# Kernel tuning notes

Hardware: AMD Instinct MI355X
Metric: run time of the kernel (lower is better)

Reference implementation:

```python
import jax, jax.numpy as jnp
import numpy as np

D_MODEL = 768
CTX_DIM = 1024
N_HEAD = 12
N_QUERIES = 256
DIM_HEAD = D_MODEL // N_HEAD  # 64
INNER = DIM_HEAD * N_HEAD     # 768
EPS = 1e-5


def layernorm(x, w, b):
    mu = jnp.mean(x, axis=-1, keepdims=True)
    var = jnp.mean((x - mu) ** 2, axis=-1, keepdims=True)
    return (x - mu) * jax.lax.rsqrt(var + EPS) * w + b


def setup_inputs() -> dict:
    key = jax.random.key(0)
    ks = jax.random.split(key, 9)
    x = jax.random.normal(ks[0], (8, 4096, CTX_DIM), dtype=jnp.float32)
    query = jax.random.normal(ks[1], (N_QUERIES, D_MODEL), dtype=jnp.float32)
    # Linear weights stored [in, out] (y = x @ W)
    Wq = jax.random.normal(ks[2], (D_MODEL, INNER), dtype=jnp.float32) * 0.02
    Wkv = jax.random.normal(ks[3], (CTX_DIM, 2 * INNER), dtype=jnp.float32) * 0.02
    Wout = jax.random.normal(ks[4], (INNER, D_MODEL), dtype=jnp.float32) * 0.02
    ln_q_w = jnp.ones((D_MODEL,), jnp.float32)
    ln_q_b = jnp.zeros((D_MODEL,), jnp.float32)
    ln_k_w = jnp.ones((CTX_DIM,), jnp.float32)
    ln_k_b = jnp.zeros((CTX_DIM,), jnp.float32)
    return {"x": x, "query": query, "ln_q_w": ln_q_w, "ln_q_b": ln_q_b,
            "ln_k_w": ln_k_w, "ln_k_b": ln_k_b, "Wq": Wq, "Wkv": Wkv, "Wout": Wout}


def reference(x, query, ln_q_w, ln_q_b, ln_k_w, ln_k_b, Wq, Wkv, Wout):
    b = x.shape[0]
    h, dh = N_HEAD, DIM_HEAD
    scale = dh ** -0.5
    xk = x[:, None]  # b 1 n d  (m = 1)
    m, n = xk.shape[1], xk.shape[2]
    q = jnp.broadcast_to(query, (b, m) + query.shape)  # b m nq d
    xk = layernorm(xk, ln_k_w, ln_k_b)
    q = layernorm(q, ln_q_w, ln_q_b)
    q = q @ Wq                          # b m nq inner
    kv = xk @ Wkv                       # b m n 2*inner
    k, v = jnp.split(kv, 2, axis=-1)
    def split_heads(t):
        bb, tt, nn, _ = t.shape
        return t.reshape(bb, tt, nn, h, dh).transpose(0, 3, 1, 2, 4)  # b h t n dh
    q, k, v = split_heads(q), split_heads(k), split_heads(v)
    sim = jnp.einsum('bhtid,bhtjd->bhtij', q * scale, k)
    attn = jax.nn.softmax(sim, axis=-1)
    out = jnp.einsum('bhtij,bhtjd->bhtid', attn, v)  # b h t nq dh
    out = out.transpose(0, 2, 3, 1, 4).reshape(b, m, N_QUERIES, INNER)
    return (out @ Wout).squeeze(axis=1)  # b nq d_model
```

## Files before the change

### kernel.cpp

```cpp
#include <hip/hip_runtime.h>
#include <hip/hip_bf16.h>
#include <math.h>

#define B_    8
#define T_    4096
#define CD    1024
#define DM    768
#define NH    12
#define DH    64
#define NQ    256
#define INNER 768
#define NKV   1536
#define MKV   (B_*T_)
#define EPS   1e-5f
#define SCALE 0.125f

typedef __attribute__((ext_vector_type(8))) short short8;
typedef __attribute__((ext_vector_type(4))) float f32x4;

__device__ __forceinline__ unsigned short f2bf(float f) {
  union { __hip_bfloat16 h; unsigned short u; } cv;
  cv.h = __float2bfloat16(f);
  return cv.u;
}

__global__ __launch_bounds__(256) void tb32_kernel(
    const float* __restrict__ src, unsigned short* __restrict__ dst,
    int Cn, int R) {
  __shared__ float tile[32][33];
  int k0 = blockIdx.x * 32, n0 = blockIdx.y * 32;
  int tid = threadIdx.x;
  int r = tid >> 3, c4 = (tid & 7) * 4;
  float4 v = *reinterpret_cast<const float4*>(&src[(size_t)(k0 + r) * Cn + n0 + c4]);
  tile[r][c4 + 0] = v.x; tile[r][c4 + 1] = v.y; tile[r][c4 + 2] = v.z; tile[r][c4 + 3] = v.w;
  __syncthreads();
  ushort4 o4;
  o4.x = f2bf(tile[c4 + 0][r]);
  o4.y = f2bf(tile[c4 + 1][r]);
  o4.z = f2bf(tile[c4 + 2][r]);
  o4.w = f2bf(tile[c4 + 3][r]);
  *reinterpret_cast<ushort4*>(&dst[(size_t)(n0 + r) * R + k0 + c4]) = o4;
}

__global__ __launch_bounds__(256) void qln_kernel(
    const float* __restrict__ query, const float* __restrict__ lnw,
    const float* __restrict__ lnb, unsigned short* __restrict__ qn) {
  int row = blockIdx.x, tid = threadIdx.x;
  __shared__ float rbuf[256];
  const float* qr = query + (size_t)row * DM;
  float v0 = qr[tid], v1 = qr[tid + 256], v2 = qr[tid + 512];
  rbuf[tid] = v0 + v1 + v2;
  __syncthreads();
  for (int o = 128; o > 0; o >>= 1) { if (tid < o) rbuf[tid] += rbuf[tid + o]; __syncthreads(); }
  float mean = rbuf[0] * (1.f / 768.f);
  __syncthreads();
  float d0 = v0 - mean, d1 = v1 - mean, d2 = v2 - mean;
  rbuf[tid] = d0 * d0 + d1 * d1 + d2 * d2;
  __syncthreads();
  for (int o = 128; o > 0; o >>= 1) { if (tid < o) rbuf[tid] += rbuf[tid + o]; __syncthreads(); }
  float var = rbuf[0] * (1.f / 768.f);
  float rs = rsqrtf(var + EPS);
  unsigned short* dst = qn + (size_t)row * DM;
  dst[tid]       = f2bf(d0 * rs * lnw[tid]       + lnb[tid]);
  dst[tid + 256] = f2bf(d1 * rs * lnw[tid + 256] + lnb[tid + 256]);
  dst[tid + 512] = f2bf(d2 * rs * lnw[tid + 512] + lnb[tid + 512]);
}

__global__ __launch_bounds__(256) void xnorm_kernel(
    const float* __restrict__ x, const float* __restrict__ lnw,
    const float* __restrict__ lnb, unsigned short* __restrict__ xn) {
  int row = blockIdx.x, tid = threadIdx.x;
  float4 v = reinterpret_cast<const float4*>(x + (size_t)row * CD)[tid];
  float s  = v.x + v.y + v.z + v.w;
  float ss = v.x * v.x + v.y * v.y + v.z * v.z + v.w * v.w;
  #pragma unroll
  for (int o = 32; o > 0; o >>= 1) { s += __shfl_down(s, o); ss += __shfl_down(ss, o); }
  __shared__ float sm[8];
  int wid = tid >> 6, lane = tid & 63;
  if (lane == 0) { sm[wid] = s; sm[4 + wid] = ss; }
  __syncthreads();
  float S  = sm[0] + sm[1] + sm[2] + sm[3];
  float SS = sm[4] + sm[5] + sm[6] + sm[7];
  float m  = S * (1.f / 1024.f);
  float var = SS * (1.f / 1024.f) - m * m;
  float rs = rsqrtf(fmaxf(var, 0.f) + EPS);
  float4 wv = reinterpret_cast<const float4*>(lnw)[tid];
  float4 bv = reinterpret_cast<const float4*>(lnb)[tid];
  ushort4 o4;
  o4.x = f2bf((v.x - m) * rs * wv.x + bv.x);
  o4.y = f2bf((v.y - m) * rs * wv.y + bv.y);
  o4.z = f2bf((v.z - m) * rs * wv.z + bv.z);
  o4.w = f2bf((v.w - m) * rs * wv.w + bv.w);
  reinterpret_cast<ushort4*>(xn + (size_t)row * CD)[tid] = o4;
}

template <int MODE>
__global__ __launch_bounds__(256) void gemm128_kernel(
    const unsigned short* __restrict__ A, const unsigned short* __restrict__ Bt,
    void* __restrict__ Cout, int N, int K, int nN, float scale, int swz) {
  __shared__ __attribute__((aligned(16))) unsigned short As[128 * 64];
  __shared__ __attribute__((aligned(16))) unsigned short Bs[128 * 64];
  int tid = threadIdx.x;
  int w = tid >> 6, lane = tid & 63;
  int bid = blockIdx.x;
  int sw = swz ? ((bid & 7) * ((int)gridDim.x >> 3) + (bid >> 3)) : bid;
  int mt = sw / nN, nt = sw % nN;
  int m0 = mt * 128, n0 = nt * 128;

  int srow[4], skoff[4];
  #pragma unroll
  for (int i = 0; i < 4; ++i) {
    int L = w * 4096 + i * 1024 + lane * 16;
    int row = L >> 7;
    int slot = (L >> 4) & 7;
    srow[i] = row;
    skoff[i] = ((slot ^ (row & 7)) << 3);
  }

  f32x4 acc[4][4];
  #pragma unroll
  for (int m = 0; m < 4; ++m)
    #pragma unroll
    for (int n = 0; n < 4; ++n) acc[m][n] = (f32x4){0.f, 0.f, 0.f, 0.f};

  int wr = w >> 1, wc = w & 1;
  int l15 = lane & 15, l4 = lane >> 4;

  for (int t = 0; t < K / 64; ++t) {
    int k0 = t * 64;
    #pragma unroll
    for (int i = 0; i < 4; ++i) {
      __builtin_amdgcn_global_load_lds(
          (const __attribute__((address_space(1))) void*)(A + (size_t)(m0 + srow[i]) * K + k0 + skoff[i]),
          (__attribute__((address_space(3))) void*)(As + w * 2048 + i * 512 + lane * 8),
          16, 0, 0);
    }
    #pragma unroll
    for (int i = 0; i < 4; ++i) {
      __builtin_amdgcn_global_load_lds(
          (const __attribute__((address_space(1))) void*)(Bt + (size_t)(n0 + srow[i]) * K + k0 + skoff[i]),
          (__attribute__((address_space(3))) void*)(Bs + w * 2048 + i * 512 + lane * 8),
          16, 0, 0);
    }
    __syncthreads();
    #pragma unroll
    for (int kh = 0; kh < 2; ++kh) {
      short8 af[4], bf[4];
      #pragma unroll
      for (int m = 0; m < 4; ++m) {
        int row = wr * 64 + m * 16 + l15;
        int byte = row * 128 + (((l4 + 4 * kh) ^ (row & 7)) << 4);
        af[m] = *reinterpret_cast<const short8*>(reinterpret_cast<const char*>(As) + byte);
      }
      #pragma unroll
      for (int n = 0; n < 4; ++n) {
        int row = wc * 64 + n * 16 + l15;
        int byte = row * 128 + (((l4 + 4 * kh) ^ (row & 7)) << 4);
        bf[n] = *reinterpret_cast<const short8*>(reinterpret_cast<const char*>(Bs) + byte);
      }
      #pragma unroll
      for (int m = 0; m < 4; ++m)
        #pragma unroll
        for (int n = 0; n < 4; ++n)
          acc[m][n] = __builtin_amdgcn_mfma_f32_16x16x32_bf16(af[m], bf[n], acc[m][n], 0, 0, 0);
    }
    __syncthreads();
  }

  #pragma unroll
  for (int m = 0; m < 4; ++m) {
    int grow = m0 + wr * 64 + m * 16 + l4 * 4;
    #pragma unroll
    for (int n = 0; n < 4; ++n) {
      int gcol = n0 + wc * 64 + n * 16 + l15;
      #pragma unroll
      for (int r = 0; r < 4; ++r) {
        if (MODE == 0)
          ((unsigned short*)Cout)[(size_t)(grow + r) * N + gcol] = f2bf(acc[m][n][r] * scale);
        else
          ((float*)Cout)[(size_t)(grow + r) * N + gcol] = acc[m][n][r];
      }
    }
  }
}

#define KBM 256
#define KBN 256
#define KBK 64
__global__ __launch_bounds__(512, 2) void kv_split_kernel(
    const unsigned short* __restrict__ xn, const unsigned short* __restrict__ wkvT,
    unsigned short* __restrict__ kvbK, unsigned short* __restrict__ vT) {
  __shared__ __attribute__((aligned(16))) unsigned short As[2][KBM * KBK];
  __shared__ __attribute__((aligned(16))) unsigned short Bs[2][KBN * KBK];
  int tid = threadIdx.x;
  int w = tid >> 6, lane = tid & 63;
  int wm = w >> 2, wn = w & 3;
  int l15 = lane & 15, l4 = lane >> 4;

  int bid = blockIdx.x;
  int sw = (bid & 7) * 96 + (bid >> 3);
  int mt = sw / (NKV / KBN), nt = sw % (NKV / KBN);
  int m0 = mt * KBM, n0 = nt * KBN;

  int srow[4], koff[4];
  #pragma unroll
  for (int i = 0; i < 4; ++i) {
    int r = i * 64 + (tid >> 3);
    srow[i] = r;
    koff[i] = (((tid & 7) ^ (r & 7)) << 3);
  }

  f32x4 acc[8][4];
  #pragma unroll
  for (int m = 0; m < 8; ++m)
    #pragma unroll
    for (int n = 0; n < 4; ++n) acc[m][n] = (f32x4){0.f, 0.f, 0.f, 0.f};

  #pragma unroll
  for (int i = 0; i < 4; ++i) {
    __builtin_amdgcn_global_load_lds(
        (const __attribute__((address_space(1))) void*)(xn + (size_t)(m0 + srow[i]) * CD + koff[i]),
        (__attribute__((address_space(3))) void*)(&As[0][0] + i * 4096 + tid * 8), 16, 0, 0);
    __builtin_amdgcn_global_load_lds(
        (const __attribute__((address_space(1))) void*)(wkvT + (size_t)(n0 + srow[i]) * CD + koff[i]),
        (__attribute__((address_space(3))) void*)(&Bs[0][0] + i * 4096 + tid * 8), 16, 0, 0);
  }
  __syncthreads();

  for (int t = 0; t < CD / KBK; ++t) {
    int cur = t & 1;
    if (t + 1 < CD / KBK) {
      int k0 = (t + 1) * KBK;
      #pragma unroll
      for (int i = 0; i < 4; ++i) {
        __builtin_amdgcn_global_load_lds(
            (const __attribute__((address_space(1))) void*)(xn + (size_t)(m0 + srow[i]) * CD + k0 + koff[i]),
            (__attribute__((address_space(3))) void*)(&As[cur ^ 1][0] + i * 4096 + tid * 8), 16, 0, 0);
        __builtin_amdgcn_global_load_lds(
            (const __attribute__((address_space(1))) void*)(wkvT + (size_t)(n0 + srow[i]) * CD + k0 + koff[i]),
            (__attribute__((address_space(3))) void*)(&Bs[cur ^ 1][0] + i * 4096 + tid * 8), 16, 0, 0);
      }
    }
    const char* Ab = reinterpret_cast<const char*>(&As[cur][0]);
    const char* Bb = reinterpret_cast<const char*>(&Bs[cur][0]);
    #pragma unroll
    for (int kh = 0; kh < 2; ++kh) {
      short8 bf[4];
      #pragma unroll
      for (int n = 0; n < 4; ++n) {
        int row = wn * 64 + n * 16 + l15;
        int byt = row * 128 + (((kh * 4 + l4) ^ (row & 7)) << 4);
        bf[n] = *reinterpret_cast<const short8*>(Bb + byt);
      }
      #pragma unroll
      for (int m = 0; m < 8; ++m) {
        int row = wm * 128 + m * 16 + l15;
        int byt = row * 128 + (((kh * 4 + l4) ^ (row & 7)) << 4);
        short8 af = *reinterpret_cast<const short8*>(Ab + byt);
        #pragma unroll
        for (int n = 0; n < 4; ++n)
          acc[m][n] = __builtin_amdgcn_mfma_f32_16x16x32_bf16(af, bf[n], acc[m][n], 0, 0, 0);
      }
    }
    __syncthreads();
  }

  if (nt < 3) {
    #pragma unroll
    for (int m = 0; m < 8; ++m) {
      int grow = m0 + wm * 128 + m * 16 + l4 * 4;
      #pragma unroll
      for (int n = 0; n < 4; ++n) {
        int gcol = nt * 256 + wn * 64 + n * 16 + l15;
        #pragma unroll
        for (int r = 0; r < 4; ++r)
          kvbK[(size_t)(grow + r) * INNER + gcol] = f2bf(acc[m][n][r]);
      }
    }
  } else {
    int b = m0 >> 12;
    int h = (nt - 3) * 4 + wn;
    #pragma unroll
    for (int m = 0; m < 8; ++m) {
      int j = (m0 & 4095) + wm * 128 + m * 16 + l4 * 4;
      #pragma unroll
      for (int n = 0; n < 4; ++n) {
        int d = n * 16 + l15;
        ushort4 o4;
        o4.x = f2bf(acc[m][n][0]); o4.y = f2bf(acc[m][n][1]);
        o4.z = f2bf(acc[m][n][2]); o4.w = f2bf(acc[m][n][3]);
        *reinterpret_cast<ushort4*>(&vT[((size_t)(b * NH + h) * DH + d) * T_ + j]) = o4;
      }
    }
  }
}

__global__ __launch_bounds__(256) void attn_mfma_kernel(
    const unsigned short* __restrict__ qpb, const unsigned short* __restrict__ kvbK,
    const unsigned short* __restrict__ vT,
    float* __restrict__ pO, float* __restrict__ pM, float* __restrict__ pL) {
  int qt = blockIdx.x, kc = blockIdx.y, bh = blockIdx.z;
  int b = bh / NH, h = bh % NH;
  __shared__ __attribute__((aligned(16))) unsigned short Ks[2][4096];
  __shared__ __attribute__((aligned(16))) unsigned short Vs[2][4096];
  __shared__ __attribute__((aligned(16))) unsigned short Ps[4][1024];
  int tid = threadIdx.x;
  int w = tid >> 6, lane = tid & 63;
  int l15 = lane & 15, l4 = lane >> 4;

  short8 qf[2];
  {
    const unsigned short* qb = qpb + (size_t)(qt * 64 + w * 16 + l15) * INNER + h * DH;
    qf[0] = *reinterpret_cast<const short8*>(qb + l4 * 8);
    qf[1] = *reinterpret_cast<const short8*>(qb + 32 + l4 * 8);
  }

  int srow0 = w * 16 + (lane >> 3);
  int srow1 = srow0 + 8;
  int koff0 = (((lane & 7) ^ (srow0 & 7)) << 3);
  int koff1 = (((lane & 7) ^ (srow1 & 7)) << 3);

  const size_t kbase = ((size_t)b * T_) * INNER + h * DH;
  const size_t vbase = ((size_t)bh * DH) * T_;

  auto stageKV = [&](int kt, int d) {
    int j0 = kc * 2048 + kt * 64;
    __builtin_amdgcn_global_load_lds(
        (const __attribute__((address_space(1))) void*)(kvbK + kbase + (size_t)(j0 + srow0) * INNER + koff0),
        (__attribute__((address_space(3))) void*)(&Ks[d][0] + w * 1024 + lane * 8), 16, 0, 0);
    __builtin_amdgcn_global_load_lds(
        (const __attribute__((address_space(1))) void*)(kvbK + kbase + (size_t)(j0 + srow1) * INNER + koff1),
        (__attribute__((address_space(3))) void*)(&Ks[d][0] + w * 1024 + 512 + lane * 8), 16, 0, 0);
    __builtin_amdgcn_global_load_lds(
        (const __attribute__((address_space(1))) void*)(vT + vbase + (size_t)srow0 * T_ + j0 + koff0),
        (__attribute__((address_space(3))) void*)(&Vs[d][0] + w * 1024 + lane * 8), 16, 0, 0);
    __builtin_amdgcn_global_load_lds(
        (const __attribute__((address_space(1))) void*)(vT + vbase + (size_t)srow1 * T_ + j0 + koff1),
        (__attribute__((address_space(3))) void*)(&Vs[d][0] + w * 1024 + 512 + lane * 8), 16, 0, 0);
  };

  f32x4 o[4];
  #pragma unroll
  for (int i = 0; i < 4; ++i) o[i] = (f32x4){0.f, 0.f, 0.f, 0.f};
  float m_run = -1e30f, l_run = 0.f;

  stageKV(0, 0);

  for (int kt = 0; kt < 32; ++kt) {
    int cur = kt & 1;
    if (kt + 1 < 32) {
      stageKV(kt + 1, cur ^ 1);
      asm volatile("s_waitcnt vmcnt(4)" ::: "memory");
    } else {
      asm volatile("s_waitcnt vmcnt(0)" ::: "memory");
    }
    __builtin_amdgcn_s_barrier();
    __builtin_amdgcn_sched_barrier(0);

    const char* Kb = reinterpret_cast<const char*>(&Ks[cur][0]);
    const char* Vb = reinterpret_cast<const char*>(&Vs[cur][0]);

    f32x4 st[4];
    __builtin_amdgcn_s_setprio(1);
    #pragma unroll
    for (int sub = 0; sub < 4; ++sub) {
      st[sub] = (f32x4){0.f, 0.f, 0.f, 0.f};
      #pragma unroll
      for (int hf = 0; hf < 2; ++hf) {
        int row = sub * 16 + l15;
        int byt = row * 128 + (((l4 + 4 * hf) ^ (row & 7)) << 4);
        short8 kf = *reinterpret_cast<const short8*>(Kb + byt);
        st[sub] = __builtin_amdgcn_mfma_f32_16x16x32_bf16(kf, qf[hf], st[sub], 0, 0, 0);
      }
    }
    __builtin_amdgcn_s_setprio(0);

    float tmax = -1e30f;
    #pragma unroll
    for (int sub = 0; sub < 4; ++sub)
      #pragma unroll
      for (int r = 0; r < 4; ++r) tmax = fmaxf(tmax, st[sub][r]);
    tmax = fmaxf(tmax, __shfl_xor(tmax, 16));
    tmax = fmaxf(tmax, __shfl_xor(tmax, 32));
    float m_new = fmaxf(m_run, tmax);
    float alpha = __expf(m_run - m_new);
    float psum = 0.f;
    #pragma unroll
    for (int sub = 0; sub < 4; ++sub) {
      float p0 = __expf(st[sub][0] - m_new);
      float p1 = __expf(st[sub][1] - m_new);
      float p2 = __expf(st[sub][2] - m_new);
      float p3 = __expf(st[sub][3] - m_new);
      psum += (p0 + p1) + (p2 + p3);
      unsigned int u0 = (unsigned int)f2bf(p0) | ((unsigned int)f2bf(p1) << 16);
      unsigned int u1 = (unsigned int)f2bf(p2) | ((unsigned int)f2bf(p3) << 16);
      int slot = (sub * 2 + (l4 >> 1)) ^ (l15 & 7);
      int byt = l15 * 128 + (slot << 4) + (l4 & 1) * 8;
      uint2 uv; uv.x = u0; uv.y = u1;
      *reinterpret_cast<uint2*>(reinterpret_cast<char*>(Ps[w]) + byt) = uv;
    }
    psum += __shfl_xor(psum, 16);
    psum += __shfl_xor(psum, 32);
    l_run = l_run * alpha + psum;
    m_run = m_new;

    float ao[4];
    #pragma unroll
    for (int r = 0; r < 4; ++r) ao[r] = __shfl(alpha, (l4 << 2) | r);
    #pragma unroll
    for (int ds = 0; ds < 4; ++ds)
      #pragma unroll
      for (int r = 0; r < 4; ++r) o[ds][r] *= ao[r];

    short8 pa[2];
    #pragma unroll
    for (int hf = 0; hf < 2; ++hf) {
      int byt = l15 * 128 + ((((hf << 2) + l4) ^ (l15 & 7)) << 4);
      pa[hf] = *reinterpret_cast<const short8*>(reinterpret_cast<const char*>(Ps[w]) + byt);
    }
    __builtin_amdgcn_s_setprio(1);
    #pragma unroll
    for (int ds = 0; ds < 4; ++ds) {
      #pragma unroll
      for (int hf = 0; hf < 2; ++hf) {
        int row = ds * 16 + l15;
        int byt = row * 128 + (((l4 + 4 * hf) ^ (row & 7)) << 4);
        short8 vf = *reinterpret_cast<const short8*>(Vb + byt);
        o[ds] = __builtin_amdgcn_mfma_f32_16x16x32_bf16(pa[hf], vf, o[ds], 0, 0, 0);
      }
    }
    __builtin_amdgcn_s_setprio(0);
    __builtin_amdgcn_s_barrier();
    __builtin_amdgcn_sched_barrier(0);
  }

  int pidx = bh * 2 + kc;
  int qrow0 = qt * 64 + w * 16;
  if (l4 == 0) {
    pM[(size_t)pidx * NQ + qrow0 + l15] = m_run;
    pL[(size_t)pidx * NQ + qrow0 + l15] = l_run;
  }
  #pragma unroll
  for (int ds = 0; ds < 4; ++ds)
    #pragma unroll
    for (int r = 0; r < 4; ++r)
      pO[((size_t)pidx * NQ + qrow0 + l4 * 4 + r) * DH + ds * 16 + l15] = o[ds][r];
}

__global__ __launch_bounds__(256) void attn_combine_kernel(
    const float* __restrict__ pO, const float* __restrict__ pM,
    const float* __restrict__ pL, unsigned short* __restrict__ attn_out) {
  int qt = blockIdx.x, bh = blockIdx.y;
  int b = bh / NH, h = bh % NH;
  int tid = threadIdx.x;
  #pragma unroll
  for (int e = 0; e < 16; ++e) {
    int idx = e * 256 + tid;
    int r = idx >> 6, d = idx & 63;
    int row = qt * 64 + r;
    size_t i0 = (size_t)(bh * 2 + 0) * NQ + row;
    size_t i1 = (size_t)(bh * 2 + 1) * NQ + row;
    float m1 = pM[i0], m2 = pM[i1], l1 = pL[i0], l2 = pL[i1];
    float M = fmaxf(m1, m2);
    float w1 = __expf(m1 - M), w2 = __expf(m2 - M);
    float L = l1 * w1 + l2 * w2;
    float oo = (pO[i0 * DH + d] * w1 + pO[i1 * DH + d] * w2) / L;
    attn_out[((size_t)b * NQ + row) * INNER + h * DH + d] = f2bf(oo);
  }
}

extern "C" void kernel_launch(void* const* d_in, const int* in_sizes, int n_in,
                              void* d_out, int out_size, void* d_ws, size_t ws_size,
                              hipStream_t stream) {
  const float* x      = (const float*)d_in[0];
  const float* query  = (const float*)d_in[1];
  const float* ln_q_w = (const float*)d_in[2];
  const float* ln_q_b = (const float*)d_in[3];
  const float* ln_k_w = (const float*)d_in[4];
  const float* ln_k_b = (const float*)d_in[5];
  const float* Wq     = (const float*)d_in[6];
  const float* Wkv    = (const float*)d_in[7];
  const float* Wout   = (const float*)d_in[8];
  float* out = (float*)d_out;

  unsigned short* qpb   = (unsigned short*)d_ws;
  unsigned short* xn    = qpb + (size_t)NQ * INNER;
  unsigned short* wkvT  = xn + (size_t)MKV * CD;
  unsigned short* kvbK  = wkvT + (size_t)NKV * CD;
  unsigned short* vT    = kvbK + (size_t)MKV * INNER;
  float* pO    = (float*)(vT + (size_t)MKV * INNER);
  float* pM    = pO + (size_t)B_ * NH * 2 * NQ * DH;
  float* pL    = pM + (size_t)B_ * NH * 2 * NQ;
  unsigned short* attnb = (unsigned short*)(pL + (size_t)B_ * NH * 2 * NQ);
  unsigned short* qn    = attnb + (size_t)B_ * NQ * INNER;
  unsigned short* WqT   = qn + (size_t)NQ * DM;
  unsigned short* WoutT = WqT + (size_t)DM * INNER;

  hipLaunchKernelGGL(tb32_kernel, dim3(CD / 32, NKV / 32), dim3(256), 0, stream,
                     Wkv, wkvT, NKV, CD);
  hipLaunchKernelGGL(tb32_kernel, dim3(DM / 32, INNER / 32), dim3(256), 0, stream,
                     Wq, WqT, INNER, DM);
  hipLaunchKernelGGL(tb32_kernel, dim3(INNER / 32, DM / 32), dim3(256), 0, stream,
                     Wout, WoutT, DM, INNER);
  hipLaunchKernelGGL(qln_kernel, dim3(NQ), dim3(256), 0, stream,
                     query, ln_q_w, ln_q_b, qn);
  hipLaunchKernelGGL((gemm128_kernel<0>), dim3((NQ / 128) * (INNER / 128)), dim3(256), 0, stream,
                     qn, WqT, (void*)qpb, INNER, DM, INNER / 128, SCALE, 0);
  hipLaunchKernelGGL(xnorm_kernel, dim3(MKV), dim3(256), 0, stream,
                     x, ln_k_w, ln_k_b, xn);
  hipLaunchKernelGGL(kv_split_kernel, dim3((MKV / KBM) * (NKV / KBN)), dim3(512), 0, stream,
                     xn, wkvT, kvbK, vT);
  hipLaunchKernelGGL(attn_mfma_kernel, dim3(4, 2, B_ * NH), dim3(256), 0, stream,
                     qpb, kvbK, vT, pO, pM, pL);
  hipLaunchKernelGGL(attn_combine_kernel, dim3(4, B_ * NH), dim3(256), 0, stream,
                     pO, pM, pL, attnb);
  hipLaunchKernelGGL((gemm128_kernel<1>), dim3((B_ * NQ / 128) * (DM / 128)), dim3(256), 0, stream,
                     attnb, WoutT, (void*)out, DM, INNER, DM / 128, 1.f, 1);
}
```

Before: 275.4 us.

## Single-buffer KV GEMM LDS for occupancy, add setprio, merge weight transposes

The KV projection GEMM drops its double-buffered LDS (64KB instead of 128KB) and raises the launch-bounds min-blocks hint to 4. The idea is to let more blocks per CU hide load latency in place of explicit in-block prefetch. MFMA sections are wrapped in s_setprio to favour the math waves. The three weight-transpose launches are merged into one z-indexed launch to cut launch overhead. Single buffering serialises load and compute inside each block. The higher occupancy target may also force register spills, given the 128 accumulator floats per thread.

Measured after the change: 938.6 us. 3.41x slower.

```diff
diff --git a/kernel.cpp b/kernel.cpp
--- a/kernel.cpp
+++ b/kernel.cpp
@@ -24,14 +24,21 @@
   return cv.u;
 }
 
-__global__ __launch_bounds__(256) void tb32_kernel(
-    const float* __restrict__ src, unsigned short* __restrict__ dst,
-    int Cn, int R) {
+__global__ __launch_bounds__(256) void tbw_kernel(
+    const float* __restrict__ s0, unsigned short* __restrict__ d0,
+    const float* __restrict__ s1, unsigned short* __restrict__ d1,
+    const float* __restrict__ s2, unsigned short* __restrict__ d2) {
+  int z = blockIdx.z;
+  const float* src; unsigned short* dst; int SR, SC;
+  if (z == 0)      { src = s0; dst = d0; SR = CD;    SC = NKV; }
+  else if (z == 1) { src = s1; dst = d1; SR = DM;    SC = INNER; }
+  else             { src = s2; dst = d2; SR = INNER; SC = DM; }
+  int k0 = blockIdx.x * 32, n0 = blockIdx.y * 32;
+  if (k0 >= SR || n0 >= SC) return;
   __shared__ float tile[32][33];
-  int k0 = blockIdx.x * 32, n0 = blockIdx.y * 32;
   int tid = threadIdx.x;
   int r = tid >> 3, c4 = (tid & 7) * 4;
-  float4 v = *reinterpret_cast<const float4*>(&src[(size_t)(k0 + r) * Cn + n0 + c4]);
+  float4 v = *reinterpret_cast<const float4*>(&src[(size_t)(k0 + r) * SC + n0 + c4]);
   tile[r][c4 + 0] = v.x; tile[r][c4 + 1] = v.y; tile[r][c4 + 2] = v.z; tile[r][c4 + 3] = v.w;
   __syncthreads();
   ushort4 o4;
@@ -39,7 +46,7 @@
   o4.y = f2bf(tile[c4 + 1][r]);
   o4.z = f2bf(tile[c4 + 2][r]);
   o4.w = f2bf(tile[c4 + 3][r]);
-  *reinterpret_cast<ushort4*>(&dst[(size_t)(n0 + r) * R + k0 + c4]) = o4;
+  *reinterpret_cast<ushort4*>(&dst[(size_t)(n0 + r) * SR + k0 + c4]) = o4;
 }
 
 __global__ __launch_bounds__(256) void qln_kernel(
@@ -187,11 +194,11 @@
 #define KBM 256
 #define KBN 256
 #define KBK 64
-__global__ __launch_bounds__(512, 2) void kv_split_kernel(
+__global__ __launch_bounds__(512, 4) void kv_split_kernel(
     const unsigned short* __restrict__ xn, const unsigned short* __restrict__ wkvT,
     unsigned short* __restrict__ kvbK, unsigned short* __restrict__ vT) {
-  __shared__ __attribute__((aligned(16))) unsigned short As[2][KBM * KBK];
-  __shared__ __attribute__((aligned(16))) unsigned short Bs[2][KBN * KBK];
+  __shared__ __attribute__((aligned(16))) unsigned short As[KBM * KBK];
+  __shared__ __attribute__((aligned(16))) unsigned short Bs[KBN * KBK];
   int tid = threadIdx.x;
   int w = tid >> 6, lane = tid & 63;
   int wm = w >> 2, wn = w & 3;
@@ -216,33 +223,20 @@
     #pragma unroll
     for (int n = 0; n < 4; ++n) acc[m][n] = (f32x4){0.f, 0.f, 0.f, 0.f};
 
-  #pragma unroll
-  for (int i = 0; i < 4; ++i) {
-    __builtin_amdgcn_global_load_lds(
-        (const __attribute__((address_space(1))) void*)(xn + (size_t)(m0 + srow[i]) * CD + koff[i]),
-        (__attribute__((address_space(3))) void*)(&As[0][0] + i * 4096 + tid * 8), 16, 0, 0);
-    __builtin_amdgcn_global_load_lds(
-        (const __attribute__((address_space(1))) void*)(wkvT + (size_t)(n0 + srow[i]) * CD + koff[i]),
-        (__attribute__((address_space(3))) void*)(&Bs[0][0] + i * 4096 + tid * 8), 16, 0, 0);
-  }
-  __syncthreads();
-
   for (int t = 0; t < CD / KBK; ++t) {
-    int cur = t & 1;
-    if (t + 1 < CD / KBK) {
-      int k0 = (t + 1) * KBK;
-      #pragma unroll
-      for (int i = 0; i < 4; ++i) {
-        __builtin_amdgcn_global_load_lds(
-            (const __attribute__((address_space(1))) void*)(xn + (size_t)(m0 + srow[i]) * CD + k0 + koff[i]),
-            (__attribute__((address_space(3))) void*)(&As[cur ^ 1][0] + i * 4096 + tid * 8), 16, 0, 0);
-        __builtin_amdgcn_global_load_lds(
-            (const __attribute__((address_space(1))) void*)(wkvT + (size_t)(n0 + srow[i]) * CD + k0 + koff[i]),
-            (__attribute__((address_space(3))) void*)(&Bs[cur ^ 1][0] + i * 4096 + tid * 8), 16, 0, 0);
-      }
-    }
-    const char* Ab = reinterpret_cast<const char*>(&As[cur][0]);
-    const char* Bb = reinterpret_cast<const char*>(&Bs[cur][0]);
+    int k0 = t * KBK;
+    #pragma unroll
+    for (int i = 0; i < 4; ++i) {
+      __builtin_amdgcn_global_load_lds(
+          (const __attribute__((address_space(1))) void*)(xn + (size_t)(m0 + srow[i]) * CD + k0 + koff[i]),
+          (__attribute__((address_space(3))) void*)(As + i * 4096 + tid * 8), 16, 0, 0);
+      __builtin_amdgcn_global_load_lds(
+          (const __attribute__((address_space(1))) void*)(wkvT + (size_t)(n0 + srow[i]) * CD + k0 + koff[i]),
+          (__attribute__((address_space(3))) void*)(Bs + i * 4096 + tid * 8), 16, 0, 0);
+    }
+    __syncthreads();
+    const char* Ab = reinterpret_cast<const char*>(As);
+    const char* Bb = reinterpret_cast<const char*>(Bs);
     #pragma unroll
     for (int kh = 0; kh < 2; ++kh) {
       short8 bf[4];
@@ -252,6 +246,7 @@
         int byt = row * 128 + (((kh * 4 + l4) ^ (row & 7)) << 4);
         bf[n] = *reinterpret_cast<const short8*>(Bb + byt);
       }
+      __builtin_amdgcn_s_setprio(1);
       #pragma unroll
       for (int m = 0; m < 8; ++m) {
         int row = wm * 128 + m * 16 + l15;
@@ -261,6 +256,7 @@
         for (int n = 0; n < 4; ++n)
           acc[m][n] = __builtin_amdgcn_mfma_f32_16x16x32_bf16(af, bf[n], acc[m][n], 0, 0, 0);
       }
+      __builtin_amdgcn_s_setprio(0);
     }
     __syncthreads();
   }
@@ -496,12 +492,8 @@
   unsigned short* WqT   = qn + (size_t)NQ * DM;
   unsigned short* WoutT = WqT + (size_t)DM * INNER;
 
-  hipLaunchKernelGGL(tb32_kernel, dim3(CD / 32, NKV / 32), dim3(256), 0, stream,
-                     Wkv, wkvT, NKV, CD);
-  hipLaunchKernelGGL(tb32_kernel, dim3(DM / 32, INNER / 32), dim3(256), 0, stream,
-                     Wq, WqT, INNER, DM);
-  hipLaunchKernelGGL(tb32_kernel, dim3(INNER / 32, DM / 32), dim3(256), 0, stream,
-                     Wout, WoutT, DM, INNER);
+  hipLaunchKernelGGL(tbw_kernel, dim3(CD / 32, NKV / 32, 3), dim3(256), 0, stream,
+                     Wkv, wkvT, Wq, WqT, Wout, WoutT);
   hipLaunchKernelGGL(qln_kernel, dim3(NQ), dim3(256), 0, stream,
                      query, ln_q_w, ln_q_b, qn);
   hipLaunchKernelGGL((gemm128_kernel<0>), dim3((NQ / 128) * (INNER / 128)), dim3(256), 0, stream,
```
